# Kernel tuning notes

Hardware: AMD Instinct MI355X
Metric: run time of the kernel (lower is better)

Reference implementation:

```python
import jax, jax.numpy as jnp
import numpy as np

# ---- fixed architecture constants (from init_kwargs) ----
N_WALL, N_ROOF, N_WINDOW = 4, 1, 2
N_RC = N_WALL + N_ROOF
HID = 32
ENC_LEN = 48
DT = 900.0
R_OPAQUE, C_OPAQUE = 10.0, 1.0e5
R_TRANS = 2.0
DIRECT_COEF, ABS_WALL_COEF, ABS_ROOF_COEF = 0.5, 0.5, 0.5
C_ZONE = 1.0e5
B, T = 2048, 1440


def setup_inputs() -> dict:
    key = jax.random.key(0)
    k0, k1, k2 = jax.random.split(key, 3)
    input_X = jax.random.normal(k0, (B, T, 7), dtype=jnp.float32)
    # EnvelopeRC deterministic inits
    rc_R_inv = jnp.concatenate([
        1.0 / (10.0 + 1.0 * jnp.arange(N_WALL, dtype=jnp.float32)),
        1.0 / (20.0 + 2.0 * jnp.arange(N_ROOF, dtype=jnp.float32))])
    rc_C_inv = jnp.concatenate([
        1.0 / (80.0 + 10.0 * jnp.arange(N_WALL, dtype=jnp.float32)),
        1.0 / (60.0 + 10.0 * jnp.arange(N_ROOF, dtype=jnp.float32))])
    window_R_inv = 1.0 / (1.0 + 0.1 * jnp.arange(N_WINDOW, dtype=jnp.float32))
    # Internal MLP: xavier_uniform with gain 0.1, zero bias
    lim1 = 0.1 * np.sqrt(6.0 / (2 + HID))
    int_W1 = jax.random.uniform(k1, (HID, 2), jnp.float32, -lim1, lim1)
    int_b1 = jnp.zeros((HID,), jnp.float32)
    lim2 = 0.1 * np.sqrt(6.0 / (HID + 1))
    int_W2 = jax.random.uniform(k2, (1, HID), jnp.float32, -lim2, lim2)
    int_b2 = jnp.zeros((1,), jnp.float32)
    return {
        'input_X': input_X,
        'rc_R_inv': rc_R_inv, 'rc_C_inv': rc_C_inv, 'window_R_inv': window_R_inv,
        'hvac_gain': jnp.float32(0.1),
        'int_W1': int_W1, 'int_b1': int_b1, 'int_W2': int_W2, 'int_b2': int_b2,
        'int_gain': jnp.float32(0.1),
        'direct_gain': jnp.float32(0.1), 'abs_wall': jnp.float32(0.1), 'abs_roof': jnp.float32(0.1),
        'zone_C_inv': jnp.float32(1.0 / 10000.0),
    }


def _forward(input_X, rc_R_inv, rc_C_inv, window_R_inv, hvac_gain,
             int_W1, int_b1, int_W2, int_b2, int_gain,
             direct_gain, abs_wall, abs_roof, zone_C_inv):
    sp = jax.nn.softplus
    Bn, Tn = input_X.shape[0], input_X.shape[1]
    tz_gt  = input_X[:, :, 0]   # [B,T]
    t_amb  = input_X[:, :, 1]
    sol    = input_X[:, :, 2]
    int_x  = input_X[:, :, 3:6]
    hvac_x = input_X[:, :, 6]

    # Internal MLP (state-free -> vectorized over time)
    h1  = jax.nn.relu(jnp.einsum('bti,hi->bth', int_x[:, :, :2], int_W1) + int_b1)
    sch = jax.nn.sigmoid(jnp.einsum('bth,oh->bto', h1, int_W2) + int_b2)[:, :, 0] + int_x[:, :, 2]
    q_int  = sp(int_gain) * 0.1 * sch          # [B,T]
    q_hvac = sp(hvac_gain) * 0.1 * hvac_x      # [B,T]

    # Bounded RC parameters
    r_inv   = sp(rc_R_inv) * (1.0 / R_OPAQUE)  # [n_rc]
    c_inv   = sp(rc_C_inv) * (1.0 / C_OPAQUE)  # [n_rc]
    win_rsum = jnp.sum(sp(window_R_inv)) * (1.0 / R_TRANS)
    abs_rc  = jnp.where(jnp.arange(N_RC) < N_WALL,
                        sp(abs_wall) * ABS_WALL_COEF,
                        sp(abs_roof) * ABS_ROOF_COEF)   # [n_rc]
    q_dir   = sp(direct_gain) * DIRECT_COEF * sol       # [B,T]
    cz_inv  = sp(zone_C_inv) * (1.0 / C_ZONE)

    # Initial state: Tmid_i = 0.7*Tzone0 + 0.3*Tamb0
    Tz0   = tz_gt[:, 0]                                      # [B]
    Tmid0 = jnp.broadcast_to((0.7 * Tz0 + 0.3 * t_amb[:, 0])[:, None], (Bn, N_RC))

    # Teacher forcing during encoder window: carry GT zone temp while t+1 < enc_len
    tz_gt_next = jnp.concatenate([tz_gt[:, 1:], tz_gt[:, -1:]], axis=1)  # [B,T]
    use_gt = (jnp.arange(Tn) + 1) < ENC_LEN                              # [T]

    xs = (t_amb.T, sol.T, q_dir.T, q_int.T, q_hvac.T, tz_gt_next.T, use_gt)

    def step(carry, x):
        Tz, Tmid = carry                      # [B], [B,n_rc]
        ta, so, qd, qi, qh, gt_next, ug = x
        q_in  = (ta[:, None] - Tmid) * r_inv
        q_out = (Tmid - Tz[:, None]) * r_inv
        dTmid = (q_in - q_out + so[:, None] * abs_rc) * c_inv
        q_env = jnp.sum(q_out, axis=1) + (ta - Tz) * win_rsum
        dTz   = (q_env + qi + qh + qd) * cz_inv
        Tz_new   = Tz + dTz * DT
        Tmid_new = Tmid + dTmid * DT
        Tz_carry = jnp.where(ug, gt_next, Tz_new)
        return (Tz_carry, Tmid_new), Tz_new

    _, tz_seq = jax.lax.scan(step, (Tz0, Tmid0), xs)   # [T,B]
    return jnp.transpose(tz_seq)[:, :, None]           # [B,T,1]


def reference(input_X, rc_R_inv, rc_C_inv, window_R_inv, hvac_gain,
              int_W1, int_b1, int_W2, int_b2, int_gain,
              direct_gain, abs_wall, abs_roof, zone_C_inv):
    return _forward(input_X, rc_R_inv, rc_C_inv, window_R_inv, hvac_gain,
                    int_W1, int_b1, int_W2, int_b2, int_gain,
                    direct_gain, abs_wall, abs_roof, zone_C_inv)
```

## Files before the change

kernel.cpp:

```cpp
#include <hip/hip_runtime.h>
#include <math.h>

#define BATCH 2048
#define TLEN  1440
#define NC    30
#define CL    48

#define PACK_OFF 0
#define E_OFF    (BATCH*TLEN*4)
#define XC_OFF   (E_OFF + NC*6*BATCH)
#define A48_OFF  (XC_OFF + BATCH*NC*6)
#define VCOL_OFF (A48_OFF + 64)
#define PRM_OFF  (VCOL_OFF + 320)
#define WS_FLOATS (PRM_OFF + 32)

__device__ __forceinline__ float sp_precise(float x) { return log1pf(expf(x)); }

__global__ void k0_params(const float* __restrict__ rcR, const float* __restrict__ rcC,
                          const float* __restrict__ winR, const float* __restrict__ hvg,
                          const float* __restrict__ ing, const float* __restrict__ dg,
                          const float* __restrict__ aw, const float* __restrict__ ar,
                          const float* __restrict__ zc, float* __restrict__ ws) {
  __shared__ float A0s[36], Ma[36], Mb[36], M16[36], vbuf[2][8];
  int ln = threadIdx.x;
  float r[5], cc[5];
  #pragma unroll
  for (int j = 0; j < 5; ++j) { r[j] = sp_precise(rcR[j]) * 0.1f; cc[j] = sp_precise(rcC[j]) * 1e-5f; }
  float w    = (sp_precise(winR[0]) + sp_precise(winR[1])) * 0.5f;
  float cz   = sp_precise(zc[0]) * 1e-5f;
  float aW   = sp_precise(aw[0]) * 0.5f, aR = sp_precise(ar[0]) * 0.5f;
  float dtcz = 900.f * cz;
  if (ln == 0) {
    float* prm = ws + PRM_OFF;
    float rsum = 0.f;
    for (int j = 0; j < 5; ++j) {
      float P = 900.f * r[j] * cc[j];
      prm[j]      = P;
      prm[5 + j]  = 1.f - 2.f * P;
      prm[10 + j] = 900.f * cc[j] * ((j < 4) ? aW : aR);
      prm[15 + j] = dtcz * r[j];
      rsum += r[j];
    }
    prm[20] = 1.f - dtcz * (w + rsum);
    prm[21] = dtcz * w;
    prm[22] = dtcz;
    prm[23] = sp_precise(ing[0]) * 0.1f;
    prm[24] = sp_precise(hvg[0]) * 0.1f;
    prm[25] = sp_precise(dg[0])  * 0.5f;
    for (int i = 0; i < 36; ++i) A0s[i] = 0.f;
    A0s[0] = prm[20];
    for (int j = 0; j < 5; ++j) {
      A0s[0 * 6 + 1 + j]       = dtcz * r[j];
      A0s[(1 + j) * 6 + 0]     = prm[j];
      A0s[(1 + j) * 6 + 1 + j] = prm[5 + j];
    }
  }
  __syncthreads();
  int i6 = ln / 6, j6 = ln % 6;
  bool act = ln < 36;
#define MM(DST, L, R) { if (act) { float s = 0.f; \
  for (int m = 0; m < 6; ++m) s = fmaf((L)[i6 * 6 + m], (R)[m * 6 + j6], s); \
  (DST)[ln] = s; } __syncthreads(); }
  MM(Mb, A0s, A0s);
  MM(Ma, Mb, Mb);
  MM(Mb, Ma, Ma);
  MM(Ma, Mb, Mb);
  if (act) M16[ln] = Ma[ln];
  __syncthreads();
  MM(Mb, Ma, Ma);
  MM(Ma, Mb, M16);
  if (act) ws[A48_OFF + ln] = Ma[ln];
  if (ln < 6) vbuf[0][ln] = A0s[ln];
  __syncthreads();
  int cur = 0;
  for (int k = 0; k < CL; ++k) {
    if (ln < 6) {
      ws[VCOL_OFF + ln * CL + k] = vbuf[cur][ln];
      float s = 0.f;
      for (int m = 0; m < 6; ++m) s = fmaf(vbuf[cur][m], A0s[m * 6 + ln], s);
      vbuf[1 - cur][ln] = s;
    }
    __syncthreads();
    cur ^= 1;
  }
}

__global__ __launch_bounds__(256) void k1_pack(const float* __restrict__ X,
    const float* __restrict__ W1, const float* __restrict__ B1,
    const float* __restrict__ W2, const float* __restrict__ B2,
    float* __restrict__ ws) {
  int tid = blockIdx.x * 256 + threadIdx.x;
  const float* prm = ws + PRM_OFF;
  float dtczw = prm[21], dtcz = prm[22], cInt = prm[23], cHv = prm[24], cDir = prm[25];
  const float* x = X + (size_t)tid * 7;
  float ta = x[1], so = x[2], x3 = x[3], x4 = x[4], x5 = x[5], hv = x[6];
  float acc = B2[0];
  #pragma unroll
  for (int h = 0; h < 32; ++h) {
    float z = fmaf(W1[2 * h], x3, fmaf(W1[2 * h + 1], x4, B1[h]));
    acc = fmaf(W2[h], fmaxf(z, 0.f), acc);
  }
  float sch = __frcp_rn(1.f + __expf(-acc)) + x5;
  float q = fmaf(cInt, sch, fmaf(cHv, hv, cDir * so));
  float u = fmaf(dtczw, ta, dtcz * q);
  int b = tid / TLEN;
  int t = tid - b * TLEN;
  float gt = (t < 47) ? x[7] : 0.f;
  ((float4*)(ws + PACK_OFF))[tid] = make_float4(ta, so, u, gt);
}

__global__ __launch_bounds__(256) void k2a_scan(const float* __restrict__ X,
                                                float* __restrict__ out,
                                                float* __restrict__ ws) {
  int tid = blockIdx.x * 256 + threadIdx.x;
  int c = tid >> 11;
  int b = tid & (BATCH - 1);
  const float* prm = ws + PRM_OFF;
  float P0 = prm[0], P1 = prm[1], P2 = prm[2], P3 = prm[3], P4 = prm[4];
  float M0 = prm[5], M1 = prm[6], M2 = prm[7], M3 = prm[8], M4 = prm[9];
  float Q0 = prm[10], Q1 = prm[11], Q2 = prm[12], Q3 = prm[13], Q4 = prm[14];
  float K0 = prm[15], K1 = prm[16], K2 = prm[17], K3 = prm[18], K4 = prm[19];
  float AZ = prm[20];
  float Tz, T0, T1, T2, T3, T4;
  bool isc0 = (c == 0);
  if (isc0) {
    float tz0 = X[(size_t)b * (TLEN * 7)];
    float ta0 = X[(size_t)b * (TLEN * 7) + 1];
    Tz = tz0;
    float tm = fmaf(0.7f, tz0, 0.3f * ta0);
    T0 = T1 = T2 = T3 = T4 = tm;
  } else {
    Tz = 0.f; T0 = T1 = T2 = T3 = T4 = 0.f;
  }
  const float4* pk = ((const float4*)(ws + PACK_OFF)) + (size_t)b * TLEN + c * CL;
  float* op = out + (size_t)b * TLEN + c * CL;
  float ob0 = 0.f, ob1 = 0.f, ob2 = 0.f, ob3 = 0.f;
  #pragma unroll 4
  for (int k = 0; k < CL; ++k) {
    float4 f = pk[k];
    float d = fmaf(K0, T0, f.z);
    d = fmaf(K1, T1, d); d = fmaf(K2, T2, d); d = fmaf(K3, T3, d); d = fmaf(K4, T4, d);
    float tzn = fmaf(AZ, Tz, d);
    T0 = fmaf(M0, T0, fmaf(P0, Tz, fmaf(P0, f.x, Q0 * f.y)));
    T1 = fmaf(M1, T1, fmaf(P1, Tz, fmaf(P1, f.x, Q1 * f.y)));
    T2 = fmaf(M2, T2, fmaf(P2, Tz, fmaf(P2, f.x, Q2 * f.y)));
    T3 = fmaf(M3, T3, fmaf(P3, Tz, fmaf(P3, f.x, Q3 * f.y)));
    T4 = fmaf(M4, T4, fmaf(P4, Tz, fmaf(P4, f.x, Q4 * f.y)));
    int ph = k & 3;
    if (ph == 0) ob0 = tzn;
    else if (ph == 1) ob1 = tzn;
    else if (ph == 2) ob2 = tzn;
    else {
      ob3 = tzn;
      ((float4*)op)[k >> 2] = make_float4(ob0, ob1, ob2, ob3);
    }
    Tz = (isc0 && k < 47) ? f.w : tzn;
  }
  float* e = ws + E_OFF + (size_t)c * 6 * BATCH + b;
  e[0] = Tz;
  e[BATCH] = T0; e[2 * BATCH] = T1; e[3 * BATCH] = T2; e[4 * BATCH] = T3; e[5 * BATCH] = T4;
}

__global__ __launch_bounds__(256) void k2b_combine(float* __restrict__ ws) {
  int b = blockIdx.x * 256 + threadIdx.x;
  __shared__ float A48s[36];
  if (threadIdx.x < 36) A48s[threadIdx.x] = ws[A48_OFF + threadIdx.x];
  __syncthreads();
  const float* e = ws + E_OFF;
  float Xs[6];
  #pragma unroll
  for (int j = 0; j < 6; ++j) Xs[j] = e[j * BATCH + b];
  float* xc = ws + XC_OFF + (size_t)b * NC * 6;
  for (int c = 1; c < NC; ++c) {
    #pragma unroll
    for (int j = 0; j < 6; ++j) xc[c * 6 + j] = Xs[j];
    if (c < NC - 1) {
      float Y[6];
      #pragma unroll
      for (int i = 0; i < 6; ++i) {
        float s = e[((size_t)c * 6 + i) * BATCH + b];
        #pragma unroll
        for (int m = 0; m < 6; ++m) s = fmaf(A48s[i * 6 + m], Xs[m], s);
        Y[i] = s;
      }
      #pragma unroll
      for (int j = 0; j < 6; ++j) Xs[j] = Y[j];
    }
  }
}

__global__ __launch_bounds__(256) void k2c_correct(float* __restrict__ out,
                                                   const float* __restrict__ ws) {
  __shared__ float V[6 * CL];
  for (int i = threadIdx.x; i < 6 * CL; i += 256) V[i] = ws[VCOL_OFF + i];
  __syncthreads();
  int tid = blockIdx.x * 256 + threadIdx.x;
  int b = tid / (TLEN - CL);
  int tt = tid - b * (TLEN - CL);
  int t = tt + CL;
  int c = t / CL;
  int kk = t - c * CL;
  const float* xc = ws + XC_OFF + ((size_t)b * NC + c) * 6;
  float s = out[(size_t)b * TLEN + t];
  #pragma unroll
  for (int j = 0; j < 6; ++j) s = fmaf(V[j * CL + kk], xc[j], s);
  out[(size_t)b * TLEN + t] = s;
}

__global__ void k_fallback(const float* __restrict__ X,
    const float* __restrict__ rcR, const float* __restrict__ rcC,
    const float* __restrict__ winR, const float* __restrict__ hvg,
    const float* __restrict__ W1, const float* __restrict__ B1,
    const float* __restrict__ W2, const float* __restrict__ B2,
    const float* __restrict__ ing, const float* __restrict__ dg,
    const float* __restrict__ aw, const float* __restrict__ ar,
    const float* __restrict__ zc, float* __restrict__ out) {
  int b = blockIdx.x * 64 + threadIdx.x;
  if (b >= BATCH) return;
  float r[5], cc[5], P[5], M[5], Q[5], K[5];
  float rsum = 0.f;
  for (int j = 0; j < 5; ++j) { r[j] = sp_precise(rcR[j]) * 0.1f; cc[j] = sp_precise(rcC[j]) * 1e-5f; rsum += r[j]; }
  float w = (sp_precise(winR[0]) + sp_precise(winR[1])) * 0.5f;
  float cz = sp_precise(zc[0]) * 1e-5f;
  float aW = sp_precise(aw[0]) * 0.5f, aR = sp_precise(ar[0]) * 0.5f;
  float dtcz = 900.f * cz;
  for (int j = 0; j < 5; ++j) {
    P[j] = 900.f * r[j] * cc[j]; M[j] = 1.f - 2.f * P[j];
    Q[j] = 900.f * cc[j] * ((j < 4) ? aW : aR); K[j] = dtcz * r[j];
  }
  float AZ = 1.f - dtcz * (w + rsum), dtczw = dtcz * w;
  float cInt = sp_precise(ing[0]) * 0.1f, cHv = sp_precise(hvg[0]) * 0.1f, cDir = sp_precise(dg[0]) * 0.5f;
  const float* xb = X + (size_t)b * (TLEN * 7);
  float Tz = xb[0];
  float tm = fmaf(0.7f, xb[0], 0.3f * xb[1]);
  float Tm[5] = {tm, tm, tm, tm, tm};
  for (int t = 0; t < TLEN; ++t) {
    const float* x = xb + t * 7;
    float ta = x[1], so = x[2], x3 = x[3], x4 = x[4], x5 = x[5], hv = x[6];
    float acc = B2[0];
    #pragma unroll
    for (int h = 0; h < 32; ++h) {
      float z = fmaf(W1[2 * h], x3, fmaf(W1[2 * h + 1], x4, B1[h]));
      acc = fmaf(W2[h], fmaxf(z, 0.f), acc);
    }
    float sch = __frcp_rn(1.f + __expf(-acc)) + x5;
    float q = fmaf(cInt, sch, fmaf(cHv, hv, cDir * so));
    float u = fmaf(dtczw, ta, dtcz * q);
    float d = u;
    #pragma unroll
    for (int j = 0; j < 5; ++j) d = fmaf(K[j], Tm[j], d);
    float tzn = fmaf(AZ, Tz, d);
    #pragma unroll
    for (int j = 0; j < 5; ++j)
      Tm[j] = fmaf(M[j], Tm[j], fmaf(P[j], Tz, fmaf(P[j], ta, Q[j] * so)));
    out[(size_t)b * TLEN + t] = tzn;
    Tz = (t < 47) ? x[7] : tzn;
  }
}

extern "C" void kernel_launch(void* const* d_in, const int* in_sizes, int n_in,
                              void* d_out, int out_size, void* d_ws, size_t ws_size,
                              hipStream_t stream) {
  const float* X    = (const float*)d_in[0];
  const float* rcR  = (const float*)d_in[1];
  const float* rcC  = (const float*)d_in[2];
  const float* winR = (const float*)d_in[3];
  const float* hvg  = (const float*)d_in[4];
  const float* W1   = (const float*)d_in[5];
  const float* B1   = (const float*)d_in[6];
  const float* W2   = (const float*)d_in[7];
  const float* B2   = (const float*)d_in[8];
  const float* ing  = (const float*)d_in[9];
  const float* dg   = (const float*)d_in[10];
  const float* aw   = (const float*)d_in[11];
  const float* ar   = (const float*)d_in[12];
  const float* zc   = (const float*)d_in[13];
  float* out = (float*)d_out;
  float* ws  = (float*)d_ws;

  if (ws_size >= (size_t)WS_FLOATS * sizeof(float)) {
    k0_params<<<1, 64, 0, stream>>>(rcR, rcC, winR, hvg, ing, dg, aw, ar, zc, ws);
    k1_pack<<<(BATCH * TLEN) / 256, 256, 0, stream>>>(X, W1, B1, W2, B2, ws);
    k2a_scan<<<(BATCH * NC) / 256, 256, 0, stream>>>(X, out, ws);
    k2b_combine<<<BATCH / 256, 256, 0, stream>>>(ws);
    k2c_correct<<<(BATCH * (TLEN - CL)) / 256, 256, 0, stream>>>(out, ws);
  } else {
    k_fallback<<<BATCH / 64, 64, 0, stream>>>(X, rcR, rcC, winR, hvg, W1, B1, W2, B2,
                                              ing, dg, aw, ar, zc, out);
  }
}
```

Baseline: 212.2 us.

## Fuse internal-MLP precompute into chunked scan kernel, dropping packed workspace

Removes the separate pack kernel that ran the internal MLP per timestep and wrote a float4 (ta, so, u, gt) array to workspace. The chunk-scan kernel now reads the raw input rows directly and computes the MLP, sigmoid and forcing term inline for each step. This saves one launch and the write plus re-read of a large packed intermediate. In exchange, the MLP work now runs on only BATCH*NC threads, serialized inside the scan loop. The strided 7-float reads per thread are also uncoalesced across threads, which risks low parallelism for that compute.

```diff
diff --git a/kernel.cpp b/kernel.cpp
--- a/kernel.cpp
+++ b/kernel.cpp
@@ -6,8 +6,7 @@
 #define NC    30
 #define CL    48
 
-#define PACK_OFF 0
-#define E_OFF    (BATCH*TLEN*4)
+#define E_OFF    0
 #define XC_OFF   (E_OFF + NC*6*BATCH)
 #define A48_OFF  (XC_OFF + BATCH*NC*6)
 #define VCOL_OFF (A48_OFF + 64)
@@ -85,33 +84,10 @@
   }
 }
 
-__global__ __launch_bounds__(256) void k1_pack(const float* __restrict__ X,
+__global__ __launch_bounds__(256) void k2a_scan(const float* __restrict__ X,
     const float* __restrict__ W1, const float* __restrict__ B1,
     const float* __restrict__ W2, const float* __restrict__ B2,
-    float* __restrict__ ws) {
-  int tid = blockIdx.x * 256 + threadIdx.x;
-  const float* prm = ws + PRM_OFF;
-  float dtczw = prm[21], dtcz = prm[22], cInt = prm[23], cHv = prm[24], cDir = prm[25];
-  const float* x = X + (size_t)tid * 7;
-  float ta = x[1], so = x[2], x3 = x[3], x4 = x[4], x5 = x[5], hv = x[6];
-  float acc = B2[0];
-  #pragma unroll
-  for (int h = 0; h < 32; ++h) {
-    float z = fmaf(W1[2 * h], x3, fmaf(W1[2 * h + 1], x4, B1[h]));
-    acc = fmaf(W2[h], fmaxf(z, 0.f), acc);
-  }
-  float sch = __frcp_rn(1.f + __expf(-acc)) + x5;
-  float q = fmaf(cInt, sch, fmaf(cHv, hv, cDir * so));
-  float u = fmaf(dtczw, ta, dtcz * q);
-  int b = tid / TLEN;
-  int t = tid - b * TLEN;
-  float gt = (t < 47) ? x[7] : 0.f;
-  ((float4*)(ws + PACK_OFF))[tid] = make_float4(ta, so, u, gt);
-}
-
-__global__ __launch_bounds__(256) void k2a_scan(const float* __restrict__ X,
-                                                float* __restrict__ out,
-                                                float* __restrict__ ws) {
+    float* __restrict__ out, float* __restrict__ ws) {
   int tid = blockIdx.x * 256 + threadIdx.x;
   int c = tid >> 11;
   int b = tid & (BATCH - 1);
@@ -121,31 +97,41 @@
   float Q0 = prm[10], Q1 = prm[11], Q2 = prm[12], Q3 = prm[13], Q4 = prm[14];
   float K0 = prm[15], K1 = prm[16], K2 = prm[17], K3 = prm[18], K4 = prm[19];
   float AZ = prm[20];
+  float dtczw = prm[21], dtcz = prm[22], cInt = prm[23], cHv = prm[24], cDir = prm[25];
+  const float* xr = X + ((size_t)b * TLEN + (size_t)c * CL) * 7;
   float Tz, T0, T1, T2, T3, T4;
   bool isc0 = (c == 0);
   if (isc0) {
-    float tz0 = X[(size_t)b * (TLEN * 7)];
-    float ta0 = X[(size_t)b * (TLEN * 7) + 1];
+    float tz0 = xr[0], ta0 = xr[1];
     Tz = tz0;
     float tm = fmaf(0.7f, tz0, 0.3f * ta0);
     T0 = T1 = T2 = T3 = T4 = tm;
   } else {
     Tz = 0.f; T0 = T1 = T2 = T3 = T4 = 0.f;
   }
-  const float4* pk = ((const float4*)(ws + PACK_OFF)) + (size_t)b * TLEN + c * CL;
   float* op = out + (size_t)b * TLEN + c * CL;
   float ob0 = 0.f, ob1 = 0.f, ob2 = 0.f, ob3 = 0.f;
   #pragma unroll 4
   for (int k = 0; k < CL; ++k) {
-    float4 f = pk[k];
-    float d = fmaf(K0, T0, f.z);
+    const float* x = xr + k * 7;
+    float ta = x[1], so = x[2], x3 = x[3], x4 = x[4], x5 = x[5], hv = x[6];
+    float acc = B2[0];
+    #pragma unroll
+    for (int h = 0; h < 32; ++h) {
+      float z = fmaf(W1[2 * h], x3, fmaf(W1[2 * h + 1], x4, B1[h]));
+      acc = fmaf(W2[h], fmaxf(z, 0.f), acc);
+    }
+    float sch = __frcp_rn(1.f + __expf(-acc)) + x5;
+    float q = fmaf(cInt, sch, fmaf(cHv, hv, cDir * so));
+    float u = fmaf(dtczw, ta, dtcz * q);
+    float d = fmaf(K0, T0, u);
     d = fmaf(K1, T1, d); d = fmaf(K2, T2, d); d = fmaf(K3, T3, d); d = fmaf(K4, T4, d);
     float tzn = fmaf(AZ, Tz, d);
-    T0 = fmaf(M0, T0, fmaf(P0, Tz, fmaf(P0, f.x, Q0 * f.y)));
-    T1 = fmaf(M1, T1, fmaf(P1, Tz, fmaf(P1, f.x, Q1 * f.y)));
-    T2 = fmaf(M2, T2, fmaf(P2, Tz, fmaf(P2, f.x, Q2 * f.y)));
-    T3 = fmaf(M3, T3, fmaf(P3, Tz, fmaf(P3, f.x, Q3 * f.y)));
-    T4 = fmaf(M4, T4, fmaf(P4, Tz, fmaf(P4, f.x, Q4 * f.y)));
+    T0 = fmaf(M0, T0, fmaf(P0, Tz, fmaf(P0, ta, Q0 * so)));
+    T1 = fmaf(M1, T1, fmaf(P1, Tz, fmaf(P1, ta, Q1 * so)));
+    T2 = fmaf(M2, T2, fmaf(P2, Tz, fmaf(P2, ta, Q2 * so)));
+    T3 = fmaf(M3, T3, fmaf(P3, Tz, fmaf(P3, ta, Q3 * so)));
+    T4 = fmaf(M4, T4, fmaf(P4, Tz, fmaf(P4, ta, Q4 * so)));
     int ph = k & 3;
     if (ph == 0) ob0 = tzn;
     else if (ph == 1) ob1 = tzn;
@@ -154,7 +140,9 @@
       ob3 = tzn;
       ((float4*)op)[k >> 2] = make_float4(ob0, ob1, ob2, ob3);
     }
-    Tz = (isc0 && k < 47) ? f.w : tzn;
+    float nz = tzn;
+    if (isc0 && k < 47) nz = x[7];
+    Tz = nz;
   }
   float* e = ws + E_OFF + (size_t)c * 6 * BATCH + b;
   e[0] = Tz;
@@ -280,8 +268,7 @@
 
   if (ws_size >= (size_t)WS_FLOATS * sizeof(float)) {
     k0_params<<<1, 64, 0, stream>>>(rcR, rcC, winR, hvg, ing, dg, aw, ar, zc, ws);
-    k1_pack<<<(BATCH * TLEN) / 256, 256, 0, stream>>>(X, W1, B1, W2, B2, ws);
-    k2a_scan<<<(BATCH * NC) / 256, 256, 0, stream>>>(X, out, ws);
+    k2a_scan<<<(BATCH * NC) / 256, 256, 0, stream>>>(X, W1, B1, W2, B2, out, ws);
     k2b_combine<<<BATCH / 256, 256, 0, stream>>>(ws);
     k2c_correct<<<(BATCH * (TLEN - CL)) / 256, 256, 0, stream>>>(out, ws);
   } else {
```

Result: slower. 223.0 us (+5.1%).
